# Optimization experiments

Hardware: AMD Instinct MI355X
Metric: run time of the kernel (lower is better)

Reference implementation:

```python
import jax, jax.numpy as jnp
import numpy as np

ALPHA = 0.3          # triplet margin
LOSS_WEIGHT = 1.0
VALID_COST = 100.0   # chosen so all queries are valid (query2gt ~ U[0,1))
POS_T = 3            # pos_thresh
NEG_T = 30           # neg_thresh
EPS = 1e-6           # torch pairwise_distance eps


def setup_inputs() -> dict:
    key0 = jax.random.key(0)
    ks = jax.random.split(key0, 6)
    Nq, V, K, D, G = 2048, 6, 4096, 256, 64
    attn = jax.random.normal(ks[0], (Nq, V, K), dtype=jnp.float32)
    query2gt = jax.random.uniform(ks[1], (Nq, G), dtype=jnp.float32)  # min < VALID_COST always
    query = jax.random.normal(ks[2], (Nq, V, D), dtype=jnp.float32)
    key = jax.random.normal(ks[3], (K, V, D), dtype=jnp.float32)
    pos_idx = jax.random.randint(ks[4], (V * Nq,), 0, POS_T, dtype=jnp.int64 if jax.config.jax_enable_x64 else jnp.int32)
    neg_idx = jax.random.randint(ks[5], (V * Nq,), POS_T, NEG_T, dtype=jnp.int64 if jax.config.jax_enable_x64 else jnp.int32)
    return {"attn": attn, "query2gt": query2gt, "query": query, "key": key,
            "pos_idx": pos_idx, "neg_idx": neg_idx}


def reference(attn, query2gt, query, key, pos_idx, neg_idx):
    # valid filtering: query2gt.min(-1) < VALID_COST is all-True by construction,
    # so no rows are dropped (keeps shapes static under jit).
    q = jnp.transpose(query, (1, 0, 2))   # [V, Nq, D]
    k = jnp.transpose(key, (1, 0, 2))     # [V, K, D]
    a = jnp.transpose(attn, (1, 0, 2))    # [V, Nq, K]
    V, Nq, K = a.shape

    # batched euclidean cdist per view via gram expansion
    qq = jnp.sum(q * q, axis=-1)[:, :, None]          # [V, Nq, 1]
    kk = jnp.sum(k * k, axis=-1)[:, None, :]          # [V, 1, K]
    d2 = qq + kk - 2.0 * jnp.einsum('vnd,vkd->vnk', q, k)
    dist = jnp.sqrt(jnp.maximum(d2, 0.0))             # [V, Nq, K]

    sorted_idx = jnp.argsort(dist, axis=-1).reshape(V * Nq, K)
    a = a.reshape(V * Nq, K)
    r = jnp.arange(V * Nq)

    pos = jax.nn.sigmoid(a[r, sorted_idx[r, pos_idx]])  # [V*Nq]
    neg = jax.nn.sigmoid(a[r, sorted_idx[r, neg_idx]])  # [V*Nq]

    # TripletMarginLoss(margin=ALPHA, p=1) with anchor = ones, 1-d embeddings
    d_pos = jnp.abs(1.0 - pos + EPS)
    d_neg = jnp.abs(1.0 - neg + EPS)
    loss = jnp.mean(jnp.maximum(d_pos - d_neg + ALPHA, 0.0))
    return LOSS_WEIGHT * loss
```

## Files before the change

kernel.cpp:

```cpp
#include <hip/hip_runtime.h>
#include <stdint.h>

#define NQ    2048
#define VV    6
#define KCNT  4096
#define DD    256
#define NROWS (VV*NQ)
#define ALPHA_M 0.3f
#define EPSL  1e-6f
#define SBIAS 256.0f

#define TM 128
#define TN 128
#define BKK 32

typedef _Float16 f16x8 __attribute__((ext_vector_type(8)));
typedef _Float16 f16x4 __attribute__((ext_vector_type(4)));
typedef float    f32x4 __attribute__((ext_vector_type(4)));

__device__ __forceinline__ void gload16(const void* g, void* l) {
    __builtin_amdgcn_global_load_lds(
        (__attribute__((address_space(1))) void*)(uintptr_t)g,
        (__attribute__((address_space(3))) void*)(uintptr_t)(uint32_t)(uintptr_t)l,
        16, 0, 0);
}

__device__ __forceinline__ unsigned ord16(_Float16 h) {
    unsigned short b = __builtin_bit_cast(unsigned short, h);
    return (b & 0x8000u) ? (unsigned)(~b & 0xFFFFu) : (unsigned)(b | 0x8000u);
}

__global__ __launch_bounds__(256) void pack_q_kernel(const float* __restrict__ query,
                                                     _Float16* __restrict__ Apack)
{
    int flat4 = blockIdx.x * 256 + threadIdx.x;
    int q   = flat4 / 384;
    int rem = flat4 - q * 384;
    int v   = rem >> 6;
    int d4  = rem & 63;
    float4 x = *(const float4*)(query + (size_t)flat4 * 4);
    f16x4 h;
    h.x = (_Float16)x.x; h.y = (_Float16)x.y;
    h.z = (_Float16)x.z; h.w = (_Float16)x.w;
    *(f16x4*)(Apack + ((size_t)(v * NQ + q)) * DD + d4 * 4) = h;
}

__global__ __launch_bounds__(256) void pack_k_kernel(const float* __restrict__ key,
                                                     _Float16* __restrict__ Bpack,
                                                     float* __restrict__ kkout)
{
    int flat4 = blockIdx.x * 256 + threadIdx.x;
    int k   = flat4 / 384;
    int rem = flat4 - k * 384;
    int v   = rem >> 6;
    int d4  = rem & 63;
    float4 x = *(const float4*)(key + (size_t)flat4 * 4);
    f16x4 h;
    h.x = (_Float16)x.x; h.y = (_Float16)x.y;
    h.z = (_Float16)x.z; h.w = (_Float16)x.w;
    *(f16x4*)(Bpack + ((size_t)(v * KCNT + k)) * DD + d4 * 4) = h;

    float s = x.x*x.x + x.y*x.y + x.z*x.z + x.w*x.w;
    #pragma unroll
    for (int off = 32; off >= 1; off >>= 1) s += __shfl_xor(s, off);
    if ((threadIdx.x & 63) == 0) kkout[v * KCNT + k] = s;
}

__global__ __launch_bounds__(256) void score_gemm(const _Float16* __restrict__ Apack,
                                                  const _Float16* __restrict__ Bpack,
                                                  const float* __restrict__ kksum,
                                                  _Float16* __restrict__ wsf,
                                                  int r0)
{
    __shared__ _Float16 As[TM * BKK];
    __shared__ _Float16 Bs[TN * BKK];

    int tid  = threadIdx.x;
    int wid  = tid >> 6;
    int lane = tid & 63;
    int c0   = blockIdx.x * TN;
    int grow = r0 + blockIdx.y * TM;
    int v    = grow / NQ;
    int q0   = grow - v * NQ;

    int srow = (wid << 4) + (lane >> 2);
    int sseg = lane & 3;
    const _Float16* Ag0 = Apack + ((size_t)(v*NQ   + q0 + srow)) * DD + sseg*8;
    const _Float16* Ag1 = Ag0 + (size_t)64 * DD;
    const _Float16* Bg0 = Bpack + ((size_t)(v*KCNT + c0 + srow)) * DD + sseg*8;
    const _Float16* Bg1 = Bg0 + (size_t)64 * DD;

    _Float16* lA0 = As + wid*512;
    _Float16* lA1 = As + 2048 + wid*512;
    _Float16* lB0 = Bs + wid*512;
    _Float16* lB1 = Bs + 2048 + wid*512;

    int fr = lane & 15;
    int kg = lane >> 4;
    int rb = (wid >> 1) * 64;
    int cb = (wid & 1) * 64;

    f32x4 acc[4][4] = {};

    for (int kb = 0; kb < DD; kb += BKK) {
        __syncthreads();
        gload16(Ag0 + kb, lA0);
        gload16(Ag1 + kb, lA1);
        gload16(Bg0 + kb, lB0);
        gload16(Bg1 + kb, lB1);
        __syncthreads();

        f16x8 af[4], bf[4];
        #pragma unroll
        for (int m = 0; m < 4; ++m)
            af[m] = *(const f16x8*)&As[(rb + m*16 + fr)*BKK + kg*8];
        #pragma unroll
        for (int n = 0; n < 4; ++n)
            bf[n] = *(const f16x8*)&Bs[(cb + n*16 + fr)*BKK + kg*8];
        #pragma unroll
        for (int m = 0; m < 4; ++m)
            #pragma unroll
            for (int n = 0; n < 4; ++n)
                acc[m][n] = __builtin_amdgcn_mfma_f32_16x16x32_f16(af[m], bf[n], acc[m][n], 0, 0, 0);
    }

    int rg = lane >> 4;
    size_t wsrow0 = (size_t)(grow - r0);
    #pragma unroll
    for (int n = 0; n < 4; ++n) {
        int C = c0 + cb + n*16 + fr;
        float kkb = kksum[v*KCNT + C] - SBIAS;
        #pragma unroll
        for (int m = 0; m < 4; ++m) {
            int Rl = rb + m*16 + rg*4;
            #pragma unroll
            for (int j = 0; j < 4; ++j)
                wsf[(wsrow0 + Rl + j) * KCNT + C] = (_Float16)(kkb - 2.0f * acc[m][n][j]);
        }
    }
}

__global__ __launch_bounds__(256) void select_kernel(const _Float16* __restrict__ wsf,
                                                     const float* __restrict__ attn,
                                                     const int* __restrict__ pos_idx,
                                                     const int* __restrict__ neg_idx,
                                                     float* __restrict__ out,
                                                     int r0)
{
    __shared__ unsigned cbuf[4][128];
    __shared__ float bsum;
    if (threadIdx.x == 0) bsum = 0.0f;
    __syncthreads();

    int wid  = threadIdx.x >> 6;
    int lane = threadIdx.x & 63;
    int lrow = blockIdx.x * 4 + wid;
    int r    = r0 + lrow;
    const _Float16* srow = wsf + (size_t)lrow * KCNT;

    f16x8 val[8];
    #pragma unroll
    for (int g = 0; g < 8; ++g)
        val[g] = *(const f16x8*)(srow + g*512 + lane*8);

    float s1 = 0.0f, s2 = 0.0f;
    #pragma unroll
    for (int g = 0; g < 8; ++g)
        #pragma unroll
        for (int j = 0; j < 8; ++j) {
            float f = (float)val[g][j];
            s1 += f; s2 += f*f;
        }
    #pragma unroll
    for (int off = 32; off >= 1; off >>= 1) {
        s1 += __shfl_xor(s1, off);
        s2 += __shfl_xor(s2, off);
    }
    float mu = s1 * (1.0f/4096.0f);
    float sd = sqrtf(fmaxf(s2 * (1.0f/4096.0f) - mu*mu, 0.0f));
    unsigned Tu = ord16((_Float16)(mu - 2.1f*sd));

    unsigned* mybuf = cbuf[wid];
    unsigned long long ltmask = (1ull << lane) - 1;
    int base = 0;
    #pragma unroll
    for (int g = 0; g < 8; ++g) {
        #pragma unroll
        for (int j = 0; j < 8; ++j) {
            unsigned ou = ord16(val[g][j]);
            bool take = ou < Tu;
            unsigned long long bal = __ballot(take);
            int pos = base + (int)__popcll(bal & ltmask);
            if (take && pos < 128)
                mybuf[pos] = (ou << 12) | (unsigned)(g*512 + lane*8 + j);
            base += (int)__popcll(bal);
        }
    }

    int p = pos_idx[r];
    int n = neg_idx[r];
    int kpos = 0, kneg = 0;

    if (base >= n + 1 && base <= 128) {
        unsigned c0 = (lane      < base) ? mybuf[lane]      : 0xFFFFFFFFu;
        unsigned c1 = (lane + 64 < base) ? mybuf[lane + 64] : 0xFFFFFFFFu;
        for (int t = 0; t <= n; ++t) {
            unsigned m = c0 < c1 ? c0 : c1;
            #pragma unroll
            for (int off = 32; off >= 1; off >>= 1) {
                unsigned o = __shfl_xor(m, off);
                m = o < m ? o : m;
            }
            if (c0 == m) c0 = 0xFFFFFFFFu;
            else if (c1 == m) c1 = 0xFFFFFFFFu;
            if (t == p) kpos = (int)(m & 0xFFFu);
            if (t == n) kneg = (int)(m & 0xFFFu);
        }
    } else {
        unsigned a[8];
        #pragma unroll
        for (int i = 0; i < 8; ++i) a[i] = 0xFFFFFFFFu;
        #pragma unroll
        for (int g = 0; g < 8; ++g)
            #pragma unroll
            for (int j = 0; j < 8; ++j) {
                unsigned key = (ord16(val[g][j]) << 12) | (unsigned)(g*512 + lane*8 + j);
                if (key < a[7]) {
                    a[7] = key;
                    #pragma unroll
                    for (int s = 7; s >= 1; --s) {
                        unsigned lo = a[s] < a[s-1] ? a[s] : a[s-1];
                        unsigned hi = a[s] < a[s-1] ? a[s-1] : a[s];
                        a[s-1] = lo; a[s] = hi;
                    }
                }
            }
        for (int t = 0; t <= n; ++t) {
            unsigned m = a[0];
            #pragma unroll
            for (int off = 32; off >= 1; off >>= 1) {
                unsigned o = __shfl_xor(m, off);
                m = o < m ? o : m;
            }
            bool win = (a[0] == m);
            #pragma unroll
            for (int s = 0; s < 7; ++s) a[s] = win ? a[s+1] : a[s];
            a[7] = win ? 0xFFFFFFFFu : a[7];
            if (t == p) kpos = (int)(m & 0xFFFu);
            if (t == n) kneg = (int)(m & 0xFFFu);
        }
    }

    if (lane == 0) {
        int v = r / NQ, q = r - v * NQ;
        float apos = attn[(size_t)q * (VV*KCNT) + v*KCNT + kpos];
        float aneg = attn[(size_t)q * (VV*KCNT) + v*KCNT + kneg];
        float pv = 1.0f / (1.0f + expf(-apos));
        float nv = 1.0f / (1.0f + expf(-aneg));
        float dp = fabsf(1.0f - pv + EPSL);
        float dn = fabsf(1.0f - nv + EPSL);
        float term = fmaxf(dp - dn + ALPHA_M, 0.0f);
        atomicAdd(&bsum, term * (1.0f / (float)NROWS));
    }
    __syncthreads();
    if (threadIdx.x == 0) atomicAdd(out, bsum);
}

extern "C" void kernel_launch(void* const* d_in, const int* in_sizes, int n_in,
                              void* d_out, int out_size, void* d_ws, size_t ws_size,
                              hipStream_t stream)
{
    const float* attn    = (const float*)d_in[0];
    const float* query   = (const float*)d_in[2];
    const float* key     = (const float*)d_in[3];
    const int*   pos_idx = (const int*)d_in[4];
    const int*   neg_idx = (const int*)d_in[5];
    float* out = (float*)d_out;

    hipMemsetAsync(d_out, 0, sizeof(float), stream);

    const size_t APACK_B = (size_t)VV * NQ   * DD * 2;
    const size_t BPACK_B = (size_t)VV * KCNT * DD * 2;
    const size_t KK_B    = (size_t)VV * KCNT * 4;
    size_t tail    = APACK_B + BPACK_B + KK_B;
    size_t tailoff = (ws_size - tail) & ~(size_t)255;

    _Float16* Apack = (_Float16*)((char*)d_ws + tailoff);
    _Float16* Bpack = (_Float16*)((char*)d_ws + tailoff + APACK_B);
    float*    kkp   = (float*)   ((char*)d_ws + tailoff + APACK_B + BPACK_B);
    _Float16* scores = (_Float16*)d_ws;

    long long cap_rows = (long long)(tailoff / ((size_t)KCNT * 2));
    long long CR = (cap_rows / TM) * TM;
    if (CR > NROWS) CR = NROWS;
    if (CR < TM)    CR = TM;

    pack_q_kernel<<<3072, 256, 0, stream>>>(query, Apack);
    pack_k_kernel<<<6144, 256, 0, stream>>>(key, Bpack, kkp);

    for (int rr0 = 0; rr0 < NROWS; rr0 += (int)CR) {
        int rows = (NROWS - rr0 < (int)CR) ? (NROWS - rr0) : (int)CR;
        dim3 gg(KCNT / TN, rows / TM);
        score_gemm<<<gg, 256, 0, stream>>>(Apack, Bpack, kkp, scores, rr0);
        select_kernel<<<rows / 4, 256, 0, stream>>>(scores, attn, pos_idx, neg_idx, out, rr0);
    }
}
```

Before: 116.8 us.

## Filter distance candidates inside GEMM epilogue using analytic per-row threshold

The full fp16 score matrix is no longer written and then re-scanned by a selection kernel. Each row now gets a threshold computed ahead of time from the key mean and norm moments (mean minus two standard deviations). The GEMM epilogue compares every score against it and appends candidates to a per-row list with atomics. A small selection kernel sorts up to 256 candidates per row, and rows whose count falls outside the valid range go to a brute-force fallback kernel. This removes about 100 MB of score traffic, but adds atomic contention in the epilogue and relies on the statistical threshold holding for most rows.

```diff
diff --git a/kernel.cpp b/kernel.cpp
--- a/kernel.cpp
+++ b/kernel.cpp
@@ -9,6 +9,8 @@
 #define ALPHA_M 0.3f
 #define EPSL  1e-6f
 #define SBIAS 256.0f
+#define ZTHR  2.0f
+#define CAP   256
 
 #define TM 128
 #define TN 128
@@ -30,47 +32,109 @@
     return (b & 0x8000u) ? (unsigned)(~b & 0xFFFFu) : (unsigned)(b | 0x8000u);
 }
 
-__global__ __launch_bounds__(256) void pack_q_kernel(const float* __restrict__ query,
-                                                     _Float16* __restrict__ Apack)
-{
-    int flat4 = blockIdx.x * 256 + threadIdx.x;
-    int q   = flat4 / 384;
-    int rem = flat4 - q * 384;
-    int v   = rem >> 6;
-    int d4  = rem & 63;
-    float4 x = *(const float4*)(query + (size_t)flat4 * 4);
+__device__ __forceinline__ float triplet_term(const float* attn, int r, int kpos, int kneg) {
+    int v = r / NQ, q = r - v * NQ;
+    float apos = attn[(size_t)q * (VV*KCNT) + v*KCNT + kpos];
+    float aneg = attn[(size_t)q * (VV*KCNT) + v*KCNT + kneg];
+    float pv = 1.0f / (1.0f + expf(-apos));
+    float nv = 1.0f / (1.0f + expf(-aneg));
+    float dp = fabsf(1.0f - pv + EPSL);
+    float dn = fabsf(1.0f - nv + EPSL);
+    return fmaxf(dp - dn + ALPHA_M, 0.0f);
+}
+
+__global__ __launch_bounds__(256) void pack_k_kernel(const float* __restrict__ key,
+                                                     _Float16* __restrict__ Bpack,
+                                                     float* __restrict__ kkp)
+{
+    int wid  = threadIdx.x >> 6;
+    int lane = threadIdx.x & 63;
+    int rowid = blockIdx.x * 4 + wid;
+    int k = rowid / 6;
+    int v = rowid - k * 6;
+    float4 x = *(const float4*)(key + (size_t)rowid * DD + lane * 4);
     f16x4 h;
     h.x = (_Float16)x.x; h.y = (_Float16)x.y;
     h.z = (_Float16)x.z; h.w = (_Float16)x.w;
-    *(f16x4*)(Apack + ((size_t)(v * NQ + q)) * DD + d4 * 4) = h;
-}
-
-__global__ __launch_bounds__(256) void pack_k_kernel(const float* __restrict__ key,
-                                                     _Float16* __restrict__ Bpack,
-                                                     float* __restrict__ kkout)
-{
-    int flat4 = blockIdx.x * 256 + threadIdx.x;
-    int k   = flat4 / 384;
-    int rem = flat4 - k * 384;
-    int v   = rem >> 6;
-    int d4  = rem & 63;
-    float4 x = *(const float4*)(key + (size_t)flat4 * 4);
+    *(f16x4*)(Bpack + ((size_t)(v * KCNT + k)) * DD + lane * 4) = h;
+
+    float s = x.x*x.x + x.y*x.y + x.z*x.z + x.w*x.w;
+    #pragma unroll
+    for (int off = 32; off >= 1; off >>= 1) s += __shfl_xor(s, off);
+    if (lane == 0) kkp[v * KCNT + k] = s;
+}
+
+__global__ __launch_bounds__(256) void kview_stats(const _Float16* __restrict__ Bpack,
+                                                   const float* __restrict__ kkp,
+                                                   float* __restrict__ kmeansum,
+                                                   float* __restrict__ kkmom)
+{
+    int v  = blockIdx.x >> 4;
+    int k0 = (blockIdx.x & 15) * 256;
+    int d  = threadIdx.x;
+
+    float macc = 0.0f;
+    for (int kk = 0; kk < 256; ++kk)
+        macc += (float)Bpack[((size_t)(v * KCNT + k0 + kk)) * DD + d];
+    atomicAdd(&kmeansum[v * DD + d], macc);
+
+    float kkval = kkp[v * KCNT + k0 + threadIdx.x];
+    float s1 = kkval, s2 = kkval * kkval;
+    #pragma unroll
+    for (int off = 32; off >= 1; off >>= 1) {
+        s1 += __shfl_xor(s1, off);
+        s2 += __shfl_xor(s2, off);
+    }
+    __shared__ float r1[4], r2[4];
+    int wid = threadIdx.x >> 6, lane = threadIdx.x & 63;
+    if (lane == 0) { r1[wid] = s1; r2[wid] = s2; }
+    __syncthreads();
+    if (threadIdx.x == 0) {
+        atomicAdd(&kkmom[2*v],   r1[0]+r1[1]+r1[2]+r1[3]);
+        atomicAdd(&kkmom[2*v+1], r2[0]+r2[1]+r2[2]+r2[3]);
+    }
+}
+
+__global__ __launch_bounds__(256) void pack_q_kernel(const float* __restrict__ query,
+                                                     _Float16* __restrict__ Apack,
+                                                     const float* __restrict__ kmeansum,
+                                                     const float* __restrict__ kkmom,
+                                                     float* __restrict__ Trow)
+{
+    int wid  = threadIdx.x >> 6;
+    int lane = threadIdx.x & 63;
+    int rowid = blockIdx.x * 4 + wid;
+    int q = rowid / 6;
+    int v = rowid - q * 6;
+    float4 x = *(const float4*)(query + (size_t)rowid * DD + lane * 4);
     f16x4 h;
     h.x = (_Float16)x.x; h.y = (_Float16)x.y;
     h.z = (_Float16)x.z; h.w = (_Float16)x.w;
-    *(f16x4*)(Bpack + ((size_t)(v * KCNT + k)) * DD + d4 * 4) = h;
-
-    float s = x.x*x.x + x.y*x.y + x.z*x.z + x.w*x.w;
-    #pragma unroll
-    for (int off = 32; off >= 1; off >>= 1) s += __shfl_xor(s, off);
-    if ((threadIdx.x & 63) == 0) kkout[v * KCNT + k] = s;
+    *(f16x4*)(Apack + ((size_t)(v * NQ + q)) * DD + lane * 4) = h;
+
+    float4 km = *(const float4*)(kmeansum + v * DD + lane * 4);
+    float qq = x.x*x.x + x.y*x.y + x.z*x.z + x.w*x.w;
+    float qk = (x.x*km.x + x.y*km.y + x.z*km.z + x.w*km.w) * (1.0f/4096.0f);
+    #pragma unroll
+    for (int off = 32; off >= 1; off >>= 1) {
+        qq += __shfl_xor(qq, off);
+        qk += __shfl_xor(qk, off);
+    }
+    if (lane == 0) {
+        float kkm = kkmom[2*v] * (1.0f/4096.0f);
+        float kkv = fmaxf(kkmom[2*v+1] * (1.0f/4096.0f) - kkm*kkm, 0.0f);
+        float mu = kkm - 2.0f * qk;
+        float sd = sqrtf(kkv + 4.0f * qq);
+        Trow[v * NQ + q] = mu - ZTHR * sd;
+    }
 }
 
 __global__ __launch_bounds__(256) void score_gemm(const _Float16* __restrict__ Apack,
                                                   const _Float16* __restrict__ Bpack,
-                                                  const float* __restrict__ kksum,
-                                                  _Float16* __restrict__ wsf,
-                                                  int r0)
+                                                  const float* __restrict__ kkp,
+                                                  const float* __restrict__ Trow,
+                                                  unsigned* __restrict__ cnt,
+                                                  unsigned* __restrict__ cand)
 {
     __shared__ _Float16 As[TM * BKK];
     __shared__ _Float16 Bs[TN * BKK];
@@ -79,7 +143,7 @@
     int wid  = tid >> 6;
     int lane = tid & 63;
     int c0   = blockIdx.x * TN;
-    int grow = r0 + blockIdx.y * TM;
+    int grow = blockIdx.y * TM;
     int v    = grow / NQ;
     int q0   = grow - v * NQ;
 
@@ -125,145 +189,143 @@
     }
 
     int rg = lane >> 4;
-    size_t wsrow0 = (size_t)(grow - r0);
-    #pragma unroll
-    for (int n = 0; n < 4; ++n) {
-        int C = c0 + cb + n*16 + fr;
-        float kkb = kksum[v*KCNT + C] - SBIAS;
+    float kkv[4];
+    #pragma unroll
+    for (int n = 0; n < 4; ++n)
+        kkv[n] = kkp[v*KCNT + c0 + cb + n*16 + fr];
+
+    #pragma unroll
+    for (int m = 0; m < 4; ++m) {
         #pragma unroll
-        for (int m = 0; m < 4; ++m) {
-            int Rl = rb + m*16 + rg*4;
+        for (int j = 0; j < 4; ++j) {
+            int gr = grow + rb + m*16 + rg*4 + j;
+            float Tr = Trow[gr];
             #pragma unroll
-            for (int j = 0; j < 4; ++j)
-                wsf[(wsrow0 + Rl + j) * KCNT + C] = (_Float16)(kkb - 2.0f * acc[m][n][j]);
-        }
-    }
-}
-
-__global__ __launch_bounds__(256) void select_kernel(const _Float16* __restrict__ wsf,
-                                                     const float* __restrict__ attn,
-                                                     const int* __restrict__ pos_idx,
-                                                     const int* __restrict__ neg_idx,
-                                                     float* __restrict__ out,
-                                                     int r0)
-{
-    __shared__ unsigned cbuf[4][128];
+            for (int n = 0; n < 4; ++n) {
+                float s = kkv[n] - 2.0f * acc[m][n][j];
+                if (s < Tr) {
+                    int C = c0 + cb + n*16 + fr;
+                    unsigned pos = atomicAdd(&cnt[gr], 1u);
+                    if (pos < CAP)
+                        cand[(size_t)gr * CAP + pos] =
+                            (ord16((_Float16)(s - SBIAS)) << 12) | (unsigned)C;
+                }
+            }
+        }
+    }
+}
+
+__global__ __launch_bounds__(256) void select2_kernel(const unsigned* __restrict__ cnt,
+                                                      const unsigned* __restrict__ cand,
+                                                      const float* __restrict__ attn,
+                                                      const int* __restrict__ pos_idx,
+                                                      const int* __restrict__ neg_idx,
+                                                      unsigned* __restrict__ fcount,
+                                                      int* __restrict__ flist,
+                                                      float* __restrict__ out)
+{
     __shared__ float bsum;
     if (threadIdx.x == 0) bsum = 0.0f;
     __syncthreads();
 
     int wid  = threadIdx.x >> 6;
     int lane = threadIdx.x & 63;
-    int lrow = blockIdx.x * 4 + wid;
-    int r    = r0 + lrow;
-    const _Float16* srow = wsf + (size_t)lrow * KCNT;
-
-    f16x8 val[8];
-    #pragma unroll
-    for (int g = 0; g < 8; ++g)
-        val[g] = *(const f16x8*)(srow + g*512 + lane*8);
-
-    float s1 = 0.0f, s2 = 0.0f;
-    #pragma unroll
-    for (int g = 0; g < 8; ++g)
-        #pragma unroll
-        for (int j = 0; j < 8; ++j) {
-            float f = (float)val[g][j];
-            s1 += f; s2 += f*f;
-        }
-    #pragma unroll
-    for (int off = 32; off >= 1; off >>= 1) {
-        s1 += __shfl_xor(s1, off);
-        s2 += __shfl_xor(s2, off);
-    }
-    float mu = s1 * (1.0f/4096.0f);
-    float sd = sqrtf(fmaxf(s2 * (1.0f/4096.0f) - mu*mu, 0.0f));
-    unsigned Tu = ord16((_Float16)(mu - 2.1f*sd));
-
-    unsigned* mybuf = cbuf[wid];
-    unsigned long long ltmask = (1ull << lane) - 1;
-    int base = 0;
-    #pragma unroll
-    for (int g = 0; g < 8; ++g) {
-        #pragma unroll
-        for (int j = 0; j < 8; ++j) {
-            unsigned ou = ord16(val[g][j]);
-            bool take = ou < Tu;
-            unsigned long long bal = __ballot(take);
-            int pos = base + (int)__popcll(bal & ltmask);
-            if (take && pos < 128)
-                mybuf[pos] = (ou << 12) | (unsigned)(g*512 + lane*8 + j);
-            base += (int)__popcll(bal);
-        }
-    }
-
+    int r    = blockIdx.x * 4 + wid;
     int p = pos_idx[r];
     int n = neg_idx[r];
-    int kpos = 0, kneg = 0;
-
-    if (base >= n + 1 && base <= 128) {
-        unsigned c0 = (lane      < base) ? mybuf[lane]      : 0xFFFFFFFFu;
-        unsigned c1 = (lane + 64 < base) ? mybuf[lane + 64] : 0xFFFFFFFFu;
+    unsigned count = cnt[r];
+
+    if (count < (unsigned)(n + 1) || count > CAP) {
+        if (lane == 0) {
+            unsigned i = atomicAdd(fcount, 1u);
+            flist[i] = r;
+        }
+    } else {
+        const unsigned* cr = cand + (size_t)r * CAP;
+        unsigned v0 = (lane       < (int)count) ? cr[lane]       : 0xFFFFFFFFu;
+        unsigned v1 = (lane + 64  < (int)count) ? cr[lane + 64]  : 0xFFFFFFFFu;
+        unsigned v2 = (lane + 128 < (int)count) ? cr[lane + 128] : 0xFFFFFFFFu;
+        unsigned v3 = (lane + 192 < (int)count) ? cr[lane + 192] : 0xFFFFFFFFu;
+        int kpos = 0, kneg = 0;
         for (int t = 0; t <= n; ++t) {
-            unsigned m = c0 < c1 ? c0 : c1;
+            unsigned m01 = v0 < v1 ? v0 : v1;
+            unsigned m23 = v2 < v3 ? v2 : v3;
+            unsigned m = m01 < m23 ? m01 : m23;
             #pragma unroll
             for (int off = 32; off >= 1; off >>= 1) {
                 unsigned o = __shfl_xor(m, off);
                 m = o < m ? o : m;
             }
-            if (c0 == m) c0 = 0xFFFFFFFFu;
-            else if (c1 == m) c1 = 0xFFFFFFFFu;
+            if      (v0 == m) v0 = 0xFFFFFFFFu;
+            else if (v1 == m) v1 = 0xFFFFFFFFu;
+            else if (v2 == m) v2 = 0xFFFFFFFFu;
+            else if (v3 == m) v3 = 0xFFFFFFFFu;
             if (t == p) kpos = (int)(m & 0xFFFu);
             if (t == n) kneg = (int)(m & 0xFFFu);
         }
-    } else {
-        unsigned a[8];
-        #pragma unroll
-        for (int i = 0; i < 8; ++i) a[i] = 0xFFFFFFFFu;
-        #pragma unroll
-        for (int g = 0; g < 8; ++g)
-            #pragma unroll
-            for (int j = 0; j < 8; ++j) {
-                unsigned key = (ord16(val[g][j]) << 12) | (unsigned)(g*512 + lane*8 + j);
-                if (key < a[7]) {
-                    a[7] = key;
-                    #pragma unroll
-                    for (int s = 7; s >= 1; --s) {
-                        unsigned lo = a[s] < a[s-1] ? a[s] : a[s-1];
-                        unsigned hi = a[s] < a[s-1] ? a[s-1] : a[s];
-                        a[s-1] = lo; a[s] = hi;
-                    }
-                }
-            }
-        for (int t = 0; t <= n; ++t) {
-            unsigned m = a[0];
-            #pragma unroll
-            for (int off = 32; off >= 1; off >>= 1) {
-                unsigned o = __shfl_xor(m, off);
-                m = o < m ? o : m;
-            }
-            bool win = (a[0] == m);
-            #pragma unroll
-            for (int s = 0; s < 7; ++s) a[s] = win ? a[s+1] : a[s];
-            a[7] = win ? 0xFFFFFFFFu : a[7];
-            if (t == p) kpos = (int)(m & 0xFFFu);
-            if (t == n) kneg = (int)(m & 0xFFFu);
-        }
-    }
-
-    if (lane == 0) {
-        int v = r / NQ, q = r - v * NQ;
-        float apos = attn[(size_t)q * (VV*KCNT) + v*KCNT + kpos];
-        float aneg = attn[(size_t)q * (VV*KCNT) + v*KCNT + kneg];
-        float pv = 1.0f / (1.0f + expf(-apos));
-        float nv = 1.0f / (1.0f + expf(-aneg));
-        float dp = fabsf(1.0f - pv + EPSL);
-        float dn = fabsf(1.0f - nv + EPSL);
-        float term = fmaxf(dp - dn + ALPHA_M, 0.0f);
-        atomicAdd(&bsum, term * (1.0f / (float)NROWS));
+        if (lane == 0)
+            atomicAdd(&bsum, triplet_term(attn, r, kpos, kneg) * (1.0f / (float)NROWS));
     }
     __syncthreads();
     if (threadIdx.x == 0) atomicAdd(out, bsum);
+}
+
+__global__ __launch_bounds__(256) void fallback_kernel(const _Float16* __restrict__ Apack,
+                                                       const _Float16* __restrict__ Bpack,
+                                                       const float* __restrict__ kkp,
+                                                       const float* __restrict__ attn,
+                                                       const int* __restrict__ pos_idx,
+                                                       const int* __restrict__ neg_idx,
+                                                       const unsigned* __restrict__ fcount,
+                                                       const int* __restrict__ flist,
+                                                       float* __restrict__ out)
+{
+    __shared__ float qrow[DD];
+    __shared__ unsigned keys[KCNT];
+    int nf = (int)*fcount;
+    for (int it = blockIdx.x; it < nf; it += gridDim.x) {
+        int r = flist[it];
+        int v = r / NQ, q = r - v * NQ;
+        qrow[threadIdx.x] = (float)Apack[((size_t)(v*NQ + q)) * DD + threadIdx.x];
+        __syncthreads();
+        for (int i = 0; i < 16; ++i) {
+            int c = i * 256 + threadIdx.x;
+            float dot = 0.0f;
+            const f16x8* bp = (const f16x8*)(Bpack + ((size_t)(v*KCNT + c)) * DD);
+            for (int d8 = 0; d8 < 32; ++d8) {
+                f16x8 b = bp[d8];
+                #pragma unroll
+                for (int j = 0; j < 8; ++j) dot += qrow[d8*8 + j] * (float)b[j];
+            }
+            float s = kkp[v*KCNT + c] - 2.0f * dot;
+            keys[c] = (ord16((_Float16)(s - SBIAS)) << 12) | (unsigned)c;
+        }
+        __syncthreads();
+        if (threadIdx.x < 64) {
+            int lane = threadIdx.x;
+            int p = pos_idx[r], n = neg_idx[r];
+            unsigned prev = 0;
+            int kpos = 0, kneg = 0;
+            for (int t = 0; t <= n; ++t) {
+                unsigned m = 0xFFFFFFFFu;
+                for (int i = 0; i < 64; ++i) {
+                    unsigned kk2 = keys[i*64 + lane];
+                    if (kk2 > prev && kk2 < m) m = kk2;
+                }
+                #pragma unroll
+                for (int off = 32; off >= 1; off >>= 1) {
+                    unsigned o = __shfl_xor(m, off);
+                    m = o < m ? o : m;
+                }
+                if (t == p) kpos = (int)(m & 0xFFFu);
+                if (t == n) kneg = (int)(m & 0xFFFu);
+                prev = m;
+            }
+            if (lane == 0)
+                atomicAdd(out, triplet_term(attn, r, kpos, kneg) * (1.0f / (float)NROWS));
+        }
+        __syncthreads();
+    }
 }
 
 extern "C" void kernel_launch(void* const* d_in, const int* in_sizes, int n_in,
@@ -277,31 +339,30 @@
     const int*   neg_idx = (const int*)d_in[5];
     float* out = (float*)d_out;
 
+    char* w = (char*)d_ws;
+    unsigned* cnt      = (unsigned*)(w);
+    float*    kmeansum = (float*)   (w + 49152);
+    float*    kkmom    = (float*)   (w + 55296);
+    unsigned* fcount   = (unsigned*)(w + 55360);
+    float*    Trow     = (float*)   (w + 55616);
+    float*    kkp      = (float*)   (w + 104768);
+    _Float16* Apack    = (_Float16*)(w + 203072);
+    _Float16* Bpack    = (_Float16*)(w + 6494528);
+    unsigned* cand     = (unsigned*)(w + 19077440);
+    int*      flist    = (int*)     (w + 31660352);
+
     hipMemsetAsync(d_out, 0, sizeof(float), stream);
-
-    const size_t APACK_B = (size_t)VV * NQ   * DD * 2;
-    const size_t BPACK_B = (size_t)VV * KCNT * DD * 2;
-    const size_t KK_B    = (size_t)VV * KCNT * 4;
-    size_t tail    = APACK_B + BPACK_B + KK_B;
-    size_t tailoff = (ws_size - tail) & ~(size_t)255;
-
-    _Float16* Apack = (_Float16*)((char*)d_ws + tailoff);
-    _Float16* Bpack = (_Float16*)((char*)d_ws + tailoff + APACK_B);
-    float*    kkp   = (float*)   ((char*)d_ws + tailoff + APACK_B + BPACK_B);
-    _Float16* scores = (_Float16*)d_ws;
-
-    long long cap_rows = (long long)(tailoff / ((size_t)KCNT * 2));
-    long long CR = (cap_rows / TM) * TM;
-    if (CR > NROWS) CR = NROWS;
-    if (CR < TM)    CR = TM;
-
-    pack_q_kernel<<<3072, 256, 0, stream>>>(query, Apack);
+    hipMemsetAsync(d_ws, 0, 55616, stream);
+
     pack_k_kernel<<<6144, 256, 0, stream>>>(key, Bpack, kkp);
-
-    for (int rr0 = 0; rr0 < NROWS; rr0 += (int)CR) {
-        int rows = (NROWS - rr0 < (int)CR) ? (NROWS - rr0) : (int)CR;
-        dim3 gg(KCNT / TN, rows / TM);
-        score_gemm<<<gg, 256, 0, stream>>>(Apack, Bpack, kkp, scores, rr0);
-        select_kernel<<<rows / 4, 256, 0, stream>>>(scores, attn, pos_idx, neg_idx, out, rr0);
-    }
-}
+    kview_stats  <<<96,   256, 0, stream>>>(Bpack, kkp, kmeansum, kkmom);
+    pack_q_kernel<<<3072, 256, 0, stream>>>(query, Apack, kmeansum, kkmom, Trow);
+
+    dim3 gg(KCNT / TN, NROWS / TM);
+    score_gemm<<<gg, 256, 0, stream>>>(Apack, Bpack, kkp, Trow, cnt, cand);
+
+    select2_kernel<<<NROWS / 4, 256, 0, stream>>>(cnt, cand, attn, pos_idx, neg_idx,
+                                                  fcount, flist, out);
+    fallback_kernel<<<64, 256, 0, stream>>>(Apack, Bpack, kkp, attn, pos_idx, neg_idx,
+                                            fcount, flist, out);
+}
```

Result: slower. 246.6 us (+111.2%).
